# Kernel optimization log

Measured on AMD Instinct MI355X. Metric: run time of the kernel, lower is better.

The kernel has to match this reference:

```python
import jax, jax.numpy as jnp
import numpy as np

N = 8192
IN_F = 512
OUT_F = 256

def setup_inputs() -> dict:
    key = jax.random.key(0)
    k1, k2, k3 = jax.random.split(key, 3)
    A = jax.random.uniform(k1, (N, N), dtype=jnp.float32)
    X = jax.random.normal(k2, (N, IN_F), dtype=jnp.float32)
    init_range = np.sqrt(6.0 / (IN_F + OUT_F)).astype(np.float32)
    W = jax.random.uniform(k3, (IN_F, OUT_F), dtype=jnp.float32,
                           minval=-init_range, maxval=init_range)
    return {"weighted_adjacency_matrix": A, "feature_matrix": X, "weight": W}

def reference(weighted_adjacency_matrix, feature_matrix, weight):
    A = weighted_adjacency_matrix
    # d = (1 + row_sum(A))^{-1/2}; D^{-1/2} A D^{-1/2} via row/col broadcast scaling
    d = jax.lax.rsqrt(1.0 + jnp.sum(A, axis=1))            # [N]
    norm_adj = d[:, None] * A * d[None, :]                  # [N, N]
    support = feature_matrix @ weight                       # [N, out_features]
    return norm_adj @ support                               # [N, out_features]
```

## Files before the change

kernel.cpp:

```cpp
#include <hip/hip_runtime.h>
#include <hip/hip_bf16.h>
#include <stdint.h>

#define NROW 8192
#define INF  512
#define OUTF 256

typedef __attribute__((ext_vector_type(8))) short bf16x8;
typedef __attribute__((ext_vector_type(4))) float f32x4;

__device__ __forceinline__ unsigned short f2bf(float x) {
  union { float f; unsigned u; } v; v.f = x;
  unsigned r = v.u + 0x7fffu + ((v.u >> 16) & 1u);
  return (unsigned short)(r >> 16);
}
__device__ __forceinline__ unsigned short f2bf_fast(float x) {
  union { float f; unsigned u; } v; v.f = x;
  return (unsigned short)((v.u + 0x8000u) >> 16);
}

__device__ __forceinline__ void async_cp16(const void* g, void* l) {
  __builtin_amdgcn_global_load_lds((const __attribute__((address_space(1))) void*)g,
                                   (__attribute__((address_space(3))) void*)l,
                                   16, 0, 0);
}

__global__ __launch_bounds__(256) void k_rowsum_convert(
    const float* __restrict__ A, unsigned short* __restrict__ Ab,
    float* __restrict__ dv) {
  int w = threadIdx.x >> 6, lane = threadIdx.x & 63;
  int row = blockIdx.x * 4 + w;
  const float4* ar = (const float4*)(A + (size_t)row * NROW);
  ushort4* br = (ushort4*)(Ab + (size_t)row * NROW);
  float s = 0.f;
  #pragma unroll 4
  for (int it = 0; it < NROW / 256; ++it) {
    float4 v = ar[it * 64 + lane];
    s += (v.x + v.y) + (v.z + v.w);
    ushort4 b;
    b.x = f2bf_fast(v.x); b.y = f2bf_fast(v.y);
    b.z = f2bf_fast(v.z); b.w = f2bf_fast(v.w);
    br[it * 64 + lane] = b;
  }
  #pragma unroll
  for (int off = 32; off > 0; off >>= 1) s += __shfl_down(s, off, 64);
  if (lane == 0) dv[row] = rsqrtf(1.f + s);
}

__global__ __launch_bounds__(256) void k_convert_x(
    const float4* __restrict__ X4, ushort4* __restrict__ Xs4) {
  int q = blockIdx.x * 256 + threadIdx.x;
  float4 v = X4[q];
  ushort4 h; h.x = f2bf(v.x); h.y = f2bf(v.y); h.z = f2bf(v.z); h.w = f2bf(v.w);
  Xs4[q] = h;
}

__global__ __launch_bounds__(256) void k_convert_w(
    const float* __restrict__ W, unsigned short* __restrict__ WsT) {
  int idx = blockIdx.x * 256 + threadIdx.x;
  int k = idx >> 8, f = idx & 255;
  WsT[(size_t)f * INF + k] = f2bf(W[idx]);
}

__global__ __launch_bounds__(256, 2) void k_support(
    const unsigned short* __restrict__ WsT,
    const unsigned short* __restrict__ Xs,
    const float* __restrict__ dv,
    unsigned short* __restrict__ YT) {
  __shared__ unsigned short lA[128 * 64];
  __shared__ unsigned short lB[128 * 64];
  const int t = threadIdx.x;
  const int w = t >> 6, lane = t & 63;
  const int m0 = blockIdx.x * 128;
  const int n0 = blockIdx.y * 128;
  const int rsub = lane >> 3, csub = lane & 7, swz = csub ^ rsub;
  const int lr = lane & 15, lq = lane >> 4, x7 = lane & 7;
  const int mw = (w >> 1) * 64, nw = (w & 1) * 64;

  f32x4 acc[4][4];
  #pragma unroll
  for (int i = 0; i < 4; ++i)
    #pragma unroll
    for (int j = 0; j < 4; ++j) acc[i][j] = f32x4{0.f, 0.f, 0.f, 0.f};

  const unsigned short* ga0 = WsT + (size_t)(m0 + w * 8 + rsub) * INF + swz * 8;
  const unsigned short* gb0 = Xs  + (size_t)(n0 + w * 8 + rsub) * INF + swz * 8;

  for (int it = 0; it < INF / 64; ++it) {
    __syncthreads();
    #pragma unroll
    for (int i = 0; i < 4; ++i) {
      async_cp16(ga0 + (size_t)(i * 32) * INF + it * 64, &lA[(i * 32 + w * 8) * 64]);
      async_cp16(gb0 + (size_t)(i * 32) * INF + it * 64, &lB[(i * 32 + w * 8) * 64]);
    }
    __syncthreads();
    #pragma unroll
    for (int ks = 0; ks < 2; ++ks) {
      bf16x8 af[4], bfv[4];
      #pragma unroll
      for (int mi = 0; mi < 4; ++mi)
        af[mi] = *(const bf16x8*)&lA[(mw + mi * 16 + lr) * 64 + (((ks * 4 + lq) ^ x7) << 3)];
      #pragma unroll
      for (int ni = 0; ni < 4; ++ni)
        bfv[ni] = *(const bf16x8*)&lB[(nw + ni * 16 + lr) * 64 + (((ks * 4 + lq) ^ x7) << 3)];
      #pragma unroll
      for (int mi = 0; mi < 4; ++mi)
        #pragma unroll
        for (int ni = 0; ni < 4; ++ni)
          acc[mi][ni] = __builtin_amdgcn_mfma_f32_16x16x32_bf16(
              af[mi], bfv[ni], acc[mi][ni], 0, 0, 0);
    }
  }
  #pragma unroll
  for (int mi = 0; mi < 4; ++mi) {
    #pragma unroll
    for (int ni = 0; ni < 4; ++ni) {
      f32x4 a = acc[mi][ni];
      int gr0 = m0 + mw + mi * 16 + lq * 4;
      int gc  = n0 + nw + ni * 16 + lr;
      float dd = dv[gc];
      #pragma unroll
      for (int r = 0; r < 4; ++r)
        YT[(size_t)(gr0 + r) * NROW + gc] = f2bf(dd * a[r]);
    }
  }
}

__global__ __launch_bounds__(256, 2) void k_gemm_main(
    const unsigned short* __restrict__ Ab,
    const unsigned short* __restrict__ YT,
    float* __restrict__ P) {
  __shared__ unsigned short lA[128 * 64];
  __shared__ unsigned short lB[256 * 64];
  const int t = threadIdx.x;
  const int w = t >> 6, lane = t & 63;
  const int m0 = blockIdx.x * 128;
  const int kz = blockIdx.y * 1024;
  const int rsub = lane >> 3, csub = lane & 7, swz = csub ^ rsub;
  const int lr = lane & 15, lq = lane >> 4, x7 = lane & 7;
  const int mw = (w & 1) * 64;
  const int nw = (w >> 1) * 128;

  f32x4 acc[4][8];
  #pragma unroll
  for (int i = 0; i < 4; ++i)
    #pragma unroll
    for (int j = 0; j < 8; ++j) acc[i][j] = f32x4{0.f, 0.f, 0.f, 0.f};

  const unsigned short* ga0 = Ab + (size_t)(m0 + w * 8 + rsub) * NROW + kz + swz * 8;
  const unsigned short* gb0 = YT + (size_t)(w * 8 + rsub) * NROW + kz + swz * 8;

  for (int it = 0; it < 16; ++it) {
    __syncthreads();
    #pragma unroll
    for (int i = 0; i < 4; ++i)
      async_cp16(ga0 + (size_t)(i * 32) * NROW + it * 64, &lA[(i * 32 + w * 8) * 64]);
    #pragma unroll
    for (int i = 0; i < 8; ++i)
      async_cp16(gb0 + (size_t)(i * 32) * NROW + it * 64, &lB[(i * 32 + w * 8) * 64]);
    __syncthreads();
    #pragma unroll
    for (int ks = 0; ks < 2; ++ks) {
      bf16x8 af[4], bfv[8];
      #pragma unroll
      for (int mi = 0; mi < 4; ++mi)
        af[mi] = *(const bf16x8*)&lA[(mw + mi * 16 + lr) * 64 + (((ks * 4 + lq) ^ x7) << 3)];
      #pragma unroll
      for (int ni = 0; ni < 8; ++ni)
        bfv[ni] = *(const bf16x8*)&lB[(nw + ni * 16 + lr) * 64 + (((ks * 4 + lq) ^ x7) << 3)];
      #pragma unroll
      for (int mi = 0; mi < 4; ++mi)
        #pragma unroll
        for (int ni = 0; ni < 8; ++ni)
          acc[mi][ni] = __builtin_amdgcn_mfma_f32_16x16x32_bf16(
              af[mi], bfv[ni], acc[mi][ni], 0, 0, 0);
    }
  }

  float* Pz = P + (size_t)blockIdx.y * NROW * OUTF;
  #pragma unroll
  for (int mi = 0; mi < 4; ++mi) {
    #pragma unroll
    for (int ni = 0; ni < 8; ++ni) {
      f32x4 a = acc[mi][ni];
      int gr0 = m0 + mw + mi * 16 + lq * 4;
      int gc  = nw + ni * 16 + lr;
      #pragma unroll
      for (int r = 0; r < 4; ++r)
        Pz[(size_t)(gr0 + r) * OUTF + gc] = a[r];
    }
  }
}

__global__ __launch_bounds__(256) void k_reduce8(
    const float4* __restrict__ P4, const float* __restrict__ dv,
    float4* __restrict__ o4) {
  int q = blockIdx.x * 256 + threadIdx.x;
  const int QT = NROW * OUTF / 4;
  float4 s = P4[q];
  #pragma unroll
  for (int z = 1; z < 8; ++z) {
    float4 v = P4[(size_t)z * QT + q];
    s.x += v.x; s.y += v.y; s.z += v.z; s.w += v.w;
  }
  float dd = dv[q >> 6];
  s.x *= dd; s.y *= dd; s.z *= dd; s.w *= dd;
  o4[q] = s;
}

__global__ __launch_bounds__(256) void k_rowsum_only(
    const float* __restrict__ A, float* __restrict__ dv) {
  int w = threadIdx.x >> 6, lane = threadIdx.x & 63;
  int row = blockIdx.x * 4 + w;
  const float4* ar = (const float4*)(A + (size_t)row * NROW);
  float s = 0.f;
  for (int it = 0; it < NROW / 256; ++it) {
    float4 v = ar[it * 64 + lane];
    s += (v.x + v.y) + (v.z + v.w);
  }
  #pragma unroll
  for (int off = 32; off > 0; off >>= 1) s += __shfl_down(s, off, 64);
  if (lane == 0) dv[row] = rsqrtf(1.f + s);
}

__global__ __launch_bounds__(256) void k_support_naive(
    const float* __restrict__ X, const float* __restrict__ W,
    const float* __restrict__ dv, float* __restrict__ Y) {
  __shared__ float lX[INF];
  int i = blockIdx.x;
  for (int k = threadIdx.x; k < INF; k += 256) lX[k] = X[(size_t)i * INF + k];
  __syncthreads();
  int f = threadIdx.x;
  float s = 0.f;
  for (int k = 0; k < INF; ++k) s += lX[k] * W[(size_t)k * OUTF + f];
  Y[(size_t)i * OUTF + f] = dv[i] * s;
}

__global__ __launch_bounds__(256) void k_main_naive(
    const float* __restrict__ A, const float* __restrict__ Y,
    const float* __restrict__ dv, float* __restrict__ out) {
  __shared__ float lA[256];
  int i = blockIdx.x, f = threadIdx.x;
  float s = 0.f;
  for (int jb = 0; jb < NROW; jb += 256) {
    __syncthreads();
    lA[threadIdx.x] = A[(size_t)i * NROW + jb + threadIdx.x];
    __syncthreads();
    for (int jj = 0; jj < 256; ++jj) s += lA[jj] * Y[(size_t)(jb + jj) * OUTF + f];
  }
  out[(size_t)i * OUTF + f] = dv[i] * s;
}

extern "C" void kernel_launch(void* const* d_in, const int* in_sizes, int n_in,
                              void* d_out, int out_size, void* d_ws, size_t ws_size,
                              hipStream_t stream) {
  const float* A = (const float*)d_in[0];
  const float* X = (const float*)d_in[1];
  const float* W = (const float*)d_in[2];
  float* out = (float*)d_out;

  const size_t SZ_AB  = (size_t)NROW * NROW * 2;
  const size_t SZ_YT  = (size_t)OUTF * NROW * 2;
  const size_t SZ_XS  = (size_t)NROW * INF * 2;
  const size_t SZ_WST = (size_t)OUTF * INF * 2;
  const size_t SZ_D   = (size_t)NROW * 4;
  const size_t SZ_P   = (size_t)8 * NROW * OUTF * 4;
  const size_t NEED = SZ_AB + SZ_YT + SZ_XS + SZ_WST + SZ_D + SZ_P;

  char* p = (char*)d_ws;
  if (ws_size >= NEED) {
    unsigned short* Ab  = (unsigned short*)p; p += SZ_AB;
    unsigned short* YT  = (unsigned short*)p; p += SZ_YT;
    unsigned short* Xs  = (unsigned short*)p; p += SZ_XS;
    unsigned short* WsT = (unsigned short*)p; p += SZ_WST;
    float* dv = (float*)p; p += SZ_D;
    float* P  = (float*)p;

    k_rowsum_convert<<<dim3(2048), dim3(256), 0, stream>>>(A, Ab, dv);
    k_convert_x<<<dim3(4096), dim3(256), 0, stream>>>((const float4*)X, (ushort4*)Xs);
    k_convert_w<<<dim3(512), dim3(256), 0, stream>>>(W, WsT);
    k_support<<<dim3(2, 64), dim3(256), 0, stream>>>(WsT, Xs, dv, YT);
    k_gemm_main<<<dim3(64, 8), dim3(256), 0, stream>>>(Ab, YT, P);
    k_reduce8<<<dim3(2048), dim3(256), 0, stream>>>((const float4*)P, dv, (float4*)out);
  } else {
    float* dv = (float*)p; p += SZ_D;
    float* Y  = (float*)p;
    k_rowsum_only<<<dim3(2048), dim3(256), 0, stream>>>(A, dv);
    k_support_naive<<<dim3(8192), dim3(256), 0, stream>>>(X, W, dv, Y);
    k_main_naive<<<dim3(8192), dim3(256), 0, stream>>>(A, Y, dv, out);
  }
}
```

Before: 460.6 us.

## Fuse X bf16 conversion into support GEMM and store split-K partials as bf16

```diff
diff --git a/kernel.cpp b/kernel.cpp
--- a/kernel.cpp
+++ b/kernel.cpp
@@ -17,6 +17,10 @@
 __device__ __forceinline__ unsigned short f2bf_fast(float x) {
   union { float f; unsigned u; } v; v.f = x;
   return (unsigned short)((v.u + 0x8000u) >> 16);
+}
+__device__ __forceinline__ float bf2f(unsigned short h) {
+  union { unsigned u; float f; } v; v.u = ((unsigned)h) << 16;
+  return v.f;
 }
 
 __device__ __forceinline__ void async_cp16(const void* g, void* l) {
@@ -47,14 +51,6 @@
   if (lane == 0) dv[row] = rsqrtf(1.f + s);
 }
 
-__global__ __launch_bounds__(256) void k_convert_x(
-    const float4* __restrict__ X4, ushort4* __restrict__ Xs4) {
-  int q = blockIdx.x * 256 + threadIdx.x;
-  float4 v = X4[q];
-  ushort4 h; h.x = f2bf(v.x); h.y = f2bf(v.y); h.z = f2bf(v.z); h.w = f2bf(v.w);
-  Xs4[q] = h;
-}
-
 __global__ __launch_bounds__(256) void k_convert_w(
     const float* __restrict__ W, unsigned short* __restrict__ WsT) {
   int idx = blockIdx.x * 256 + threadIdx.x;
@@ -62,9 +58,9 @@
   WsT[(size_t)f * INF + k] = f2bf(W[idx]);
 }
 
-__global__ __launch_bounds__(256, 2) void k_support(
+__global__ __launch_bounds__(256, 2) void k_support_fx(
     const unsigned short* __restrict__ WsT,
-    const unsigned short* __restrict__ Xs,
+    const float* __restrict__ X,
     const float* __restrict__ dv,
     unsigned short* __restrict__ YT) {
   __shared__ unsigned short lA[128 * 64];
@@ -77,6 +73,9 @@
   const int lr = lane & 15, lq = lane >> 4, x7 = lane & 7;
   const int mw = (w >> 1) * 64, nw = (w & 1) * 64;
 
+  const int xrow = t >> 1, xhalf = t & 1;
+  const float4* xsrc = (const float4*)(X + (size_t)(n0 + xrow) * INF + xhalf * 32);
+
   f32x4 acc[4][4];
   #pragma unroll
   for (int i = 0; i < 4; ++i)
@@ -84,14 +83,21 @@
     for (int j = 0; j < 4; ++j) acc[i][j] = f32x4{0.f, 0.f, 0.f, 0.f};
 
   const unsigned short* ga0 = WsT + (size_t)(m0 + w * 8 + rsub) * INF + swz * 8;
-  const unsigned short* gb0 = Xs  + (size_t)(n0 + w * 8 + rsub) * INF + swz * 8;
 
   for (int it = 0; it < INF / 64; ++it) {
     __syncthreads();
     #pragma unroll
-    for (int i = 0; i < 4; ++i) {
+    for (int i = 0; i < 4; ++i)
       async_cp16(ga0 + (size_t)(i * 32) * INF + it * 64, &lA[(i * 32 + w * 8) * 64]);
-      async_cp16(gb0 + (size_t)(i * 32) * INF + it * 64, &lB[(i * 32 + w * 8) * 64]);
+    #pragma unroll
+    for (int u = 0; u < 8; ++u) {
+      float4 v = xsrc[it * 16 + u];
+      ushort4 b;
+      b.x = f2bf(v.x); b.y = f2bf(v.y); b.z = f2bf(v.z); b.w = f2bf(v.w);
+      int k = xhalf * 32 + u * 4;
+      int chunk = k >> 3, klo = k & 7;
+      int slot = chunk ^ (xrow & 7);
+      *(ushort4*)&lB[xrow * 64 + (slot << 3) + klo] = b;
     }
     __syncthreads();
     #pragma unroll
@@ -129,7 +135,7 @@
 __global__ __launch_bounds__(256, 2) void k_gemm_main(
     const unsigned short* __restrict__ Ab,
     const unsigned short* __restrict__ YT,
-    float* __restrict__ P) {
+    unsigned short* __restrict__ P) {
   __shared__ unsigned short lA[128 * 64];
   __shared__ unsigned short lB[256 * 64];
   const int t = threadIdx.x;
@@ -177,7 +183,7 @@
     }
   }
 
-  float* Pz = P + (size_t)blockIdx.y * NROW * OUTF;
+  unsigned short* Pz = P + (size_t)blockIdx.y * NROW * OUTF;
   #pragma unroll
   for (int mi = 0; mi < 4; ++mi) {
     #pragma unroll
@@ -187,21 +193,21 @@
       int gc  = nw + ni * 16 + lr;
       #pragma unroll
       for (int r = 0; r < 4; ++r)
-        Pz[(size_t)(gr0 + r) * OUTF + gc] = a[r];
+        Pz[(size_t)(gr0 + r) * OUTF + gc] = f2bf_fast(a[r]);
     }
   }
 }
 
 __global__ __launch_bounds__(256) void k_reduce8(
-    const float4* __restrict__ P4, const float* __restrict__ dv,
+    const ushort4* __restrict__ P4, const float* __restrict__ dv,
     float4* __restrict__ o4) {
   int q = blockIdx.x * 256 + threadIdx.x;
   const int QT = NROW * OUTF / 4;
-  float4 s = P4[q];
-  #pragma unroll
-  for (int z = 1; z < 8; ++z) {
-    float4 v = P4[(size_t)z * QT + q];
-    s.x += v.x; s.y += v.y; s.z += v.z; s.w += v.w;
+  float4 s = {0.f, 0.f, 0.f, 0.f};
+  #pragma unroll
+  for (int z = 0; z < 8; ++z) {
+    ushort4 v = P4[(size_t)z * QT + q];
+    s.x += bf2f(v.x); s.y += bf2f(v.y); s.z += bf2f(v.z); s.w += bf2f(v.w);
   }
   float dd = dv[q >> 6];
   s.x *= dd; s.y *= dd; s.z *= dd; s.w *= dd;
@@ -261,27 +267,24 @@
 
   const size_t SZ_AB  = (size_t)NROW * NROW * 2;
   const size_t SZ_YT  = (size_t)OUTF * NROW * 2;
-  const size_t SZ_XS  = (size_t)NROW * INF * 2;
   const size_t SZ_WST = (size_t)OUTF * INF * 2;
   const size_t SZ_D   = (size_t)NROW * 4;
-  const size_t SZ_P   = (size_t)8 * NROW * OUTF * 4;
-  const size_t NEED = SZ_AB + SZ_YT + SZ_XS + SZ_WST + SZ_D + SZ_P;
+  const size_t SZ_P   = (size_t)8 * NROW * OUTF * 2;
+  const size_t NEED = SZ_AB + SZ_YT + SZ_WST + SZ_D + SZ_P;
 
   char* p = (char*)d_ws;
   if (ws_size >= NEED) {
     unsigned short* Ab  = (unsigned short*)p; p += SZ_AB;
     unsigned short* YT  = (unsigned short*)p; p += SZ_YT;
-    unsigned short* Xs  = (unsigned short*)p; p += SZ_XS;
     unsigned short* WsT = (unsigned short*)p; p += SZ_WST;
     float* dv = (float*)p; p += SZ_D;
-    float* P  = (float*)p;
+    unsigned short* P = (unsigned short*)p;
 
     k_rowsum_convert<<<dim3(2048), dim3(256), 0, stream>>>(A, Ab, dv);
-    k_convert_x<<<dim3(4096), dim3(256), 0, stream>>>((const float4*)X, (ushort4*)Xs);
     k_convert_w<<<dim3(512), dim3(256), 0, stream>>>(W, WsT);
-    k_support<<<dim3(2, 64), dim3(256), 0, stream>>>(WsT, Xs, dv, YT);
+    k_support_fx<<<dim3(2, 64), dim3(256), 0, stream>>>(WsT, X, dv, YT);
     k_gemm_main<<<dim3(64, 8), dim3(256), 0, stream>>>(Ab, YT, P);
-    k_reduce8<<<dim3(2048), dim3(256), 0, stream>>>((const float4*)P, dv, (float4*)out);
+    k_reduce8<<<dim3(2048), dim3(256), 0, stream>>>((const ushort4*)P, dv, (float4*)out);
   } else {
     float* dv = (float*)p; p += SZ_D;
     float* Y  = (float*)p;
```

New measurement: 457.4 us. About the same (-0.7%).
